# Performance work log

Hardware: AMD Instinct MI355X
Metric: run time of the kernel (lower is better)

## Reference

```python
import jax, jax.numpy as jnp
import numpy as np
from jax import lax

BIN_NUM = 48
CPG = BIN_NUM * 3            # 144 hidden channels
NOUT = BIN_NUM + 1           # 49 symbols
K = 5                        # masked conv kernel size
H, W = 256, 512
TABLE_TOTAL = 65536.0        # EntropyTable total frequency
SCALE = 2.0 / (BIN_NUM - 1.0)


def _causal_mask(include_center: bool) -> jnp.ndarray:
    # Raster-scan causal 5x5 mask: all rows above center, left of center in
    # center row; center tap only for 'hidden' (mask-B) layers.
    m = np.zeros((K, K), np.float32)
    c = K // 2
    m[:c, :] = 1.0
    m[c, :c] = 1.0
    if include_center:
        m[c, c] = 1.0
    return jnp.asarray(m)[None, None]  # broadcast over (O, I, kh, kw)


def _mconv(x, w, b, mask):
    # x: (N, C, H, W); w: (O, I, K, K)
    y = lax.conv_general_dilated(
        x, w * mask, window_strides=(1, 1), padding='SAME',
        dimension_numbers=('NCHW', 'OIHW', 'NCHW'))
    return y + b[None, :, None, None]


def setup_inputs() -> dict:
    key = jax.random.key(0)
    ks = jax.random.split(key, 8)
    # quantized code indices in [0, BIN_NUM)
    data = jax.random.randint(ks[0], (1, 1, H, W), 0, BIN_NUM).astype(jnp.float32)
    s0 = 1.0 / np.sqrt(1 * K * K)
    sr = 1.0 / np.sqrt(CPG * K * K)
    w0 = jax.random.normal(ks[1], (CPG, 1, K, K), jnp.float32) * s0
    b0 = jnp.zeros((CPG,), jnp.float32)
    # 5 residual blocks x 2 convs = 10 hidden masked convs, stacked
    wres = jax.random.normal(ks[2], (10, CPG, CPG, K, K), jnp.float32) * sr
    bres = jnp.zeros((10, CPG), jnp.float32)
    wl = jax.random.normal(ks[3], (NOUT, CPG, K, K), jnp.float32) * sr
    bl = jnp.zeros((NOUT,), jnp.float32)
    return {"data": data, "w0": w0, "b0": b0, "wres": wres, "bres": bres,
            "wl": wl, "bl": bl}


def reference(data, w0, b0, wres, bres, wl, bl):
    mask_a = _causal_mask(False)   # first layer excludes center pixel
    mask_b = _causal_mask(True)    # hidden layers include center pixel

    # Scale(-1, 2/(bin_num-1)): map codes [0, bin_num-1] -> [-1, 1]
    x = data * SCALE - 1.0
    x = jax.nn.relu(_mconv(x, w0, b0, mask_a))
    # 5 residual blocks: y = relu(conv(relu(conv(x)))) + x
    for i in range(5):
        h1 = jax.nn.relu(_mconv(x, wres[2 * i], bres[2 * i], mask_b))
        h2 = jax.nn.relu(_mconv(h1, wres[2 * i + 1], bres[2 * i + 1], mask_b))
        x = x + h2
    logits = _mconv(x, wl, bl, mask_b)          # (1, 49, H, W)

    # EntropyTable: per-pixel softmax -> cumulative frequency table (total 65536)
    probs = jax.nn.softmax(logits, axis=1)
    cdf = jnp.cumsum(probs, axis=1) * TABLE_TOTAL
    zeros = jnp.zeros((cdf.shape[0], 1) + cdf.shape[2:], cdf.dtype)
    vec = jnp.concatenate([zeros, cdf], axis=1)  # (1, 50, H, W)
    return vec
```

## Files before the change

kernel.cpp:

```cpp
#include <hip/hip_runtime.h>

#define HH 256
#define WW 512
#define CPG 144
#define NCO 192
#define NKG 18
#define WP 516
#define HPADR 258
#define XB_E ((size_t)NKG * HPADR * WP * 8)
#define NCH 59
#define KREAL 1872
#define SCALE_F (2.0f / 47.0f)

typedef __attribute__((ext_vector_type(8))) short short8;
typedef __attribute__((ext_vector_type(4))) float floatx4;

__device__ __forceinline__ unsigned short f2bf(float f) {
    unsigned u = __builtin_bit_cast(unsigned, f);
    u += 0x7FFFu + ((u >> 16) & 1u);
    return (unsigned short)(u >> 16);
}
__device__ __forceinline__ float bf2f(unsigned short h) {
    unsigned u = ((unsigned)h) << 16;
    return __builtin_bit_cast(float, u);
}
__device__ __forceinline__ void async16(const void* g, void* l) {
    __builtin_amdgcn_global_load_lds(
        (const __attribute__((address_space(1))) unsigned int*)g,
        (__attribute__((address_space(3))) unsigned int*)l, 16, 0, 0);
}
__device__ __forceinline__ void tap_decode(int t, int& kh, int& kw) {
    kh = t < 5 ? 0 : (t < 10 ? 1 : 2);
    kw = t - (t < 5 ? 0 : (t < 10 ? 5 : 10));
}
__device__ __forceinline__ unsigned aoff68(int c, int lg) {
    int g = c * 4 + lg;
    if (g > 233) g = 233;
    int t = (g * 57) >> 10;
    int kgp = g - t * 18;
    int kh, kw; tap_decode(t, kh, kw);
    return (unsigned)(((kgp * 4 + kh) * 68 + kw) * 16);
}
__device__ __forceinline__ unsigned aoff132(int c, int lg) {
    int g = c * 4 + lg;
    if (g > 233) g = 233;
    int t = (g * 57) >> 10;
    int kgp = g - t * 18;
    int kh, kw; tap_decode(t, kh, kw);
    return (unsigned)(((kgp * 4 + kh) * 132 + kw) * 16);
}

__global__ void k_zero(float* __restrict__ p, size_t n4) {
    size_t i = (size_t)blockIdx.x * blockDim.x + threadIdx.x;
    size_t stride = (size_t)gridDim.x * blockDim.x;
    float4 z = make_float4(0.f, 0.f, 0.f, 0.f);
    for (; i < n4; i += stride) ((float4*)p)[i] = z;
}

__global__ void k_pack_hidden(const float* __restrict__ wres, unsigned short* __restrict__ wpk) {
    const int total = 10 * NCH * NCO * 32;
    int i = blockIdx.x * blockDim.x + threadIdx.x;
    int stride = gridDim.x * blockDim.x;
    for (; i < total; i += stride) {
        int kk = i & 31;
        int q  = i >> 5;
        int co = q % NCO;  q /= NCO;
        int c  = q % NCH;
        int l  = q / NCH;
        int K = c * 32 + kk;
        float v = 0.f;
        if (K < KREAL && co < CPG) {
            int t = K / CPG, ci = K - t * CPG;
            int kh, kw; tap_decode(t, kh, kw);
            v = wres[(((size_t)(l * CPG + co) * CPG + ci) * 5 + kh) * 5 + kw];
        }
        wpk[i] = f2bf(v);
    }
}
__global__ void k_pack_final(const float* __restrict__ wl, unsigned short* __restrict__ wpkF) {
    const int total = NCH * 64 * 32;
    int i = blockIdx.x * blockDim.x + threadIdx.x;
    if (i >= total) return;
    int kk = i & 31;
    int co = (i >> 5) & 63;
    int c  = i >> 11;
    int K = c * 32 + kk;
    float v = 0.f;
    if (K < KREAL && co < 49) {
        int t = K / CPG, ci = K - t * CPG;
        int kh, kw; tap_decode(t, kh, kw);
        v = wl[(((size_t)co * CPG + ci) * 5 + kh) * 5 + kw];
    }
    wpkF[i] = f2bf(v);
}
__global__ void k_pack_small(const float* __restrict__ w0, const float* __restrict__ bl,
                             float* __restrict__ w0p, float* __restrict__ blp) {
    int i = blockIdx.x * blockDim.x + threadIdx.x;
    if (i < 12 * CPG) {
        int co = i % CPG, t = i / CPG;
        int kh, kw; tap_decode(t, kh, kw);
        w0p[i] = w0[co * 25 + kh * 5 + kw];
    } else if (i < 12 * CPG + 64) {
        int k = i - 12 * CPG;
        blp[k] = k < 49 ? bl[k] : 0.f;
    }
}

__global__ __launch_bounds__(384) void k_layer0(
    const float* __restrict__ data, const float* __restrict__ w0p,
    const float* __restrict__ b0, unsigned short* __restrict__ Xb) {
    const int lane = threadIdx.x;
    const int x = blockIdx.x * 64 + lane;
    const int y = blockIdx.y;

    float xv[12];
#pragma unroll
    for (int t = 0; t < 12; t++) {
        int kh, kw; tap_decode(t, kh, kw);
        int yy = y + kh - 2, xx = x + kw - 2;
        xv[t] = (yy >= 0 && xx >= 0 && xx < WW) ? data[yy * WW + xx] * SCALE_F - 1.0f : 0.f;
    }
#pragma unroll
    for (int kgi = 0; kgi < 3; kgi++) {
        int kg = threadIdx.y * 3 + kgi;
        float a8[8];
#pragma unroll
        for (int j = 0; j < 8; j++) a8[j] = 0.f;
#pragma unroll
        for (int t = 0; t < 12; t++)
#pragma unroll
            for (int j = 0; j < 8; j++)
                a8[j] = fmaf(w0p[t * CPG + kg * 8 + j], xv[t], a8[j]);
        short8 o;
#pragma unroll
        for (int j = 0; j < 8; j++)
            o[j] = (short)f2bf(fmaxf(a8[j] + b0[kg * 8 + j], 0.f));
        *(short8*)&Xb[((size_t)(kg * HPADR + y + 2) * WP + (x + 2)) * 8] = o;
    }
}

template<bool RES>
__global__ __launch_bounds__(512, 4) void k_conv(
    const unsigned short* __restrict__ in,
    const unsigned short* __restrict__ wq,
    const float* __restrict__ bias,
    const unsigned short* __restrict__ res,
    unsigned short* __restrict__ out) {
    __shared__ __align__(16) unsigned short As[NKG][4][68][8];
    const int tid  = threadIdx.x;
    const int lane = tid & 63;
    const int wid  = tid >> 6;
    const int ng   = wid & 3;
    const int r    = wid >> 2;
    const int lr = lane & 15;
    const int lg = lane >> 4;

    const int fid = blockIdx.x + (int)gridDim.x * blockIdx.y;
    const int swz = (fid & 7) * 128 + (fid >> 3);
    const int x0 = (swz & 7) * 64;
    const int y0 = (swz >> 3) * 2;

    floatx4 acc[4][3];
#pragma unroll
    for (int m = 0; m < 4; m++)
#pragma unroll
        for (int n = 0; n < 3; n++) acc[m][n] = (floatx4)0.f;

    for (int i = wid; i < 72; i += 8) {
        int rr = i & 3;
        int kg = i >> 2;
        async16(in + ((size_t)(kg * HPADR + y0 + rr) * WP + x0 + lane) * 8,
                &As[kg][rr][0][0]);
    }
    if (tid < 288) {
        int kg = tid >> 4;
        int rr = (tid >> 2) & 3;
        int p  = tid & 3;
        *(short8*)&As[kg][rr][64 + p][0] =
            *(const short8*)(in + ((size_t)(kg * HPADR + y0 + rr) * WP + x0 + 64 + p) * 8);
    }
    asm volatile("s_waitcnt vmcnt(0) lgkmcnt(0)" ::: "memory");
    __builtin_amdgcn_s_barrier();
    __builtin_amdgcn_sched_barrier(0);

    const char* abase = (const char*)As + ((size_t)(r * 68) + lr) * 16;
    auto LDA = [&](int c, short8 (&a)[4]) {
        const char* ap = abase + aoff68(c, lg);
#pragma unroll
        for (int m = 0; m < 4; ++m) a[m] = *(const short8*)(ap + m * 256);
    };
    auto LDB = [&](int c, short8 (&b)[3]) {
        const unsigned short* bp = wq + (size_t)c * (NCO * 32) + (ng * 48 + lr) * 32 + lg * 8;
#pragma unroll
        for (int n = 0; n < 3; ++n) b[n] = *(const short8*)(bp + n * 512);
    };
    auto CMP = [&](const short8 (&a)[4], const short8 (&b)[3]) {
        __builtin_amdgcn_sched_barrier(0);
        __builtin_amdgcn_s_setprio(1);
#pragma unroll
        for (int m = 0; m < 4; ++m)
#pragma unroll
            for (int n = 0; n < 3; ++n)
                acc[m][n] = __builtin_amdgcn_mfma_f32_16x16x32_bf16(a[m], b[n], acc[m][n], 0, 0, 0);
        __builtin_amdgcn_s_setprio(0);
        __builtin_amdgcn_sched_barrier(0);
    };

    short8 A0[4], A1[4], B0[3], B1[3];
    LDB(0, B0); LDA(0, A0);
#pragma unroll 1
    for (int c = 0; c < 56; c += 2) {
        LDB(c + 1, B1); LDA(c + 1, A1);
        CMP(A0, B0);
        LDB(c + 2, B0); LDA(c + 2, A0);
        CMP(A1, B1);
    }
    LDB(57, B1); LDA(57, A1);
    CMP(A0, B0);
    LDB(58, B0); LDA(58, A0);
    CMP(A1, B1);
    CMP(A0, B0);

    if (ng < 3) {
#pragma unroll
        for (int n = 0; n < 3; ++n) {
            int co = ng * 48 + n * 16 + lr;
            float bv = bias[co];
            const size_t pb = ((size_t)((co >> 3) * HPADR + y0 + 2 + r) * WP + (x0 + 2)) * 8 + (co & 7);
#pragma unroll
            for (int m = 0; m < 4; ++m)
#pragma unroll
                for (int rr = 0; rr < 4; ++rr) {
                    int px = m * 16 + lg * 4 + rr;
                    size_t o = pb + (size_t)px * 8;
                    float v = fmaxf(acc[m][n][rr] + bv, 0.f);
                    if (RES) v += bf2f(res[o]);
                    out[o] = f2bf(v);
                }
        }
    }
}

__global__ __launch_bounds__(512, 2) void k_logits(
    const unsigned short* __restrict__ in,
    const unsigned short* __restrict__ wq,
    const float* __restrict__ blp,
    float* __restrict__ logits) {
    __shared__ __align__(16) unsigned short As[NKG][4][132][8];
    const int tid  = threadIdx.x;
    const int lane = tid & 63;
    const int wid  = tid >> 6;
    const int ng   = wid & 1;
    const int r    = (wid >> 1) & 1;
    const int ph   = wid >> 2;
    const int lr = lane & 15;
    const int lg = lane >> 4;

    const int fid = blockIdx.x + (int)gridDim.x * blockIdx.y;
    const int swz = (fid & 7) * 64 + (fid >> 3);
    const int x0 = (swz & 3) * 128;
    const int y0 = (swz >> 2) * 2;

    floatx4 acc[4][2];
#pragma unroll
    for (int m = 0; m < 4; m++)
#pragma unroll
        for (int n = 0; n < 2; n++) acc[m][n] = (floatx4)0.f;

    for (int i = wid; i < 144; i += 8) {
        int half = i & 1;
        int rr   = (i >> 1) & 3;
        int kg   = i >> 3;
        async16(in + ((size_t)(kg * HPADR + y0 + rr) * WP + x0 + half * 64 + lane) * 8,
                &As[kg][rr][half * 64][0]);
    }
    if (tid < 288) {
        int kg = tid >> 4;
        int rr = (tid >> 2) & 3;
        int pxl = 128 + (tid & 3);
        *(short8*)&As[kg][rr][pxl][0] =
            *(const short8*)(in + ((size_t)(kg * HPADR + y0 + rr) * WP + x0 + pxl) * 8);
    }
    asm volatile("s_waitcnt vmcnt(0) lgkmcnt(0)" ::: "memory");
    __builtin_amdgcn_s_barrier();
    __builtin_amdgcn_sched_barrier(0);

    const char* abase = (const char*)As + ((size_t)(r * 132) + ph * 64 + lr) * 16;
    auto LDA = [&](int c, short8 (&a)[4]) {
        const char* ap = abase + aoff132(c, lg);
#pragma unroll
        for (int m = 0; m < 4; ++m) a[m] = *(const short8*)(ap + m * 256);
    };
    auto LDB = [&](int c, short8 (&b)[2]) {
        const unsigned short* bp = wq + (size_t)c * 2048 + (ng * 32 + lr) * 32 + lg * 8;
#pragma unroll
        for (int n = 0; n < 2; ++n) b[n] = *(const short8*)(bp + n * 512);
    };
    auto CMP = [&](const short8 (&a)[4], const short8 (&b)[2]) {
        __builtin_amdgcn_sched_barrier(0);
        __builtin_amdgcn_s_setprio(1);
#pragma unroll
        for (int m = 0; m < 4; ++m)
#pragma unroll
            for (int n = 0; n < 2; ++n)
                acc[m][n] = __builtin_amdgcn_mfma_f32_16x16x32_bf16(a[m], b[n], acc[m][n], 0, 0, 0);
        __builtin_amdgcn_s_setprio(0);
        __builtin_amdgcn_sched_barrier(0);
    };

    short8 A0[4], A1[4], B0[2], B1[2], B2[2], B3[2];
    LDB(0, B0); LDB(1, B1); LDA(0, A0);
#pragma unroll 1
    for (int c = 0; c < 56; c += 4) {
        LDB(c + 2, B2); LDB(c + 3, B3);
        LDA(c + 1, A1); CMP(A0, B0);
        LDA(c + 2, A0); CMP(A1, B1);
        LDB(c + 4, B0); LDB(c + 5, B1);
        LDA(c + 3, A1); CMP(A0, B2);
        LDA(c + 4, A0); CMP(A1, B3);
    }
    LDB(58, B2);
    LDA(57, A1); CMP(A0, B0);
    LDA(58, A0); CMP(A1, B1);
    CMP(A0, B2);

#pragma unroll
    for (int n = 0; n < 2; ++n) {
        int co = ng * 32 + n * 16 + lr;
        float bv = blp[co];
#pragma unroll
        for (int m = 0; m < 4; ++m)
#pragma unroll
            for (int rr = 0; rr < 4; ++rr) {
                int px = ph * 64 + m * 16 + lg * 4 + rr;
                logits[((size_t)(y0 + r) * WW + x0 + px) * 64 + co] = acc[m][n][rr] + bv;
            }
    }
}

__global__ __launch_bounds__(256) void k_softmax(
    const float* __restrict__ lg, float* __restrict__ out) {
    const int px = blockIdx.x * 256 + threadIdx.x;
    const int y = blockIdx.y;
    const size_t p = (size_t)y * WW + px;
    const float* l = lg + p * 64;
    float v[49];
    float m = -1e30f;
#pragma unroll
    for (int k = 0; k < 49; k++) { v[k] = l[k]; m = fmaxf(m, v[k]); }
    float s = 0.f;
#pragma unroll
    for (int k = 0; k < 49; k++) {
        v[k] = exp2f((v[k] - m) * 1.44269504088896f);
        s += v[k];
    }
    const float inv = 65536.0f / s;
    out[p] = 0.f;
    float run = 0.f;
#pragma unroll
    for (int k = 0; k < 49; k++) {
        run += v[k];
        out[(size_t)(k + 1) * (HH * WW) + p] = run * inv;
    }
}

extern "C" void kernel_launch(void* const* d_in, const int* in_sizes, int n_in,
                              void* d_out, int out_size, void* d_ws, size_t ws_size,
                              hipStream_t stream) {
    (void)in_sizes; (void)n_in; (void)out_size; (void)ws_size;
    const float* data = (const float*)d_in[0];
    const float* w0   = (const float*)d_in[1];
    const float* b0   = (const float*)d_in[2];
    const float* wres = (const float*)d_in[3];
    const float* bres = (const float*)d_in[4];
    const float* wl   = (const float*)d_in[5];
    const float* bl   = (const float*)d_in[6];
    float* out = (float*)d_out;

    char* ws = (char*)d_ws;
    unsigned short* Xb   = (unsigned short*)ws;
    unsigned short* Hb   = Xb + XB_E;
    unsigned short* wpk  = Hb + XB_E;
    unsigned short* wpkF = wpk + (size_t)10 * NCH * NCO * 32;
    float* blp  = (float*)(wpkF + (size_t)NCH * 64 * 32);
    float* w0p  = blp + 64;
    float* logits = w0p + 1728;

    k_zero<<<2048, 256, 0, stream>>>((float*)ws, (2 * XB_E * 2) / 16);

    k_pack_hidden<<<2048, 256, 0, stream>>>(wres, wpk);
    k_pack_final<<<(NCH * 64 * 32 + 255) / 256, 256, 0, stream>>>(wl, wpkF);
    k_pack_small<<<7, 256, 0, stream>>>(w0, bl, w0p, blp);

    k_layer0<<<dim3(8, 256), dim3(64, 6), 0, stream>>>(data, w0p, b0, Xb);

    const size_t LSTRIDE = (size_t)NCH * NCO * 32;
    for (int i = 0; i < 5; i++) {
        k_conv<false><<<dim3(8, 128), 512, 0, stream>>>(
            Xb, wpk + (size_t)(2 * i) * LSTRIDE, bres + (2 * i) * CPG, Xb, Hb);
        k_conv<true><<<dim3(8, 128), 512, 0, stream>>>(
            Hb, wpk + (size_t)(2 * i + 1) * LSTRIDE, bres + (2 * i + 1) * CPG, Xb, Xb);
    }

    k_logits<<<dim3(4, 128), 512, 0, stream>>>(Xb, wpkF, blp, logits);
    k_softmax<<<dim3(2, 256), 256, 0, stream>>>(logits, out);
}
```

Before: 1.046 ms.

## Stage conv weights in LDS ring buffer and enlarge tile to four rows

The hidden-layer conv kernel now covers four output rows per block with twelve waves (768 threads), removing the idle fourth channel-group of waves by dropping the padding to 192 output channels. Weights are repacked without that padding and streamed through a 3-slot LDS ring using async global-to-LDS loads, so waves in a block share the weight reads instead of each fetching from global memory. The cost is a block barrier every K-chunk, more LDS per block and lower occupancy (3 blocks of 768 threads).

```diff
diff --git a/kernel.cpp b/kernel.cpp
--- a/kernel.cpp
+++ b/kernel.cpp
@@ -3,7 +3,6 @@
 #define HH 256
 #define WW 512
 #define CPG 144
-#define NCO 192
 #define NKG 18
 #define WP 516
 #define HPADR 258
@@ -12,6 +11,9 @@
 #define KREAL 1872
 #define SCALE_F (2.0f / 47.0f)
 
+#define BSLAB 1552
+#define BSLOT (4 * BSLAB)
+
 typedef __attribute__((ext_vector_type(8))) short short8;
 typedef __attribute__((ext_vector_type(4))) float floatx4;
 
@@ -33,13 +35,13 @@
     kh = t < 5 ? 0 : (t < 10 ? 1 : 2);
     kw = t - (t < 5 ? 0 : (t < 10 ? 5 : 10));
 }
-__device__ __forceinline__ unsigned aoff68(int c, int lg) {
+__device__ __forceinline__ unsigned aoff6(int c, int lg) {
     int g = c * 4 + lg;
     if (g > 233) g = 233;
     int t = (g * 57) >> 10;
     int kgp = g - t * 18;
     int kh, kw; tap_decode(t, kh, kw);
-    return (unsigned)(((kgp * 4 + kh) * 68 + kw) * 16);
+    return (unsigned)(((kgp * 6 + kh) * 68 + kw) * 16);
 }
 __device__ __forceinline__ unsigned aoff132(int c, int lg) {
     int g = c * 4 + lg;
@@ -58,18 +60,19 @@
 }
 
 __global__ void k_pack_hidden(const float* __restrict__ wres, unsigned short* __restrict__ wpk) {
-    const int total = 10 * NCH * NCO * 32;
+    const int total = 10 * NCH * 4 * CPG * 8;
     int i = blockIdx.x * blockDim.x + threadIdx.x;
     int stride = gridDim.x * blockDim.x;
     for (; i < total; i += stride) {
-        int kk = i & 31;
-        int q  = i >> 5;
-        int co = q % NCO;  q /= NCO;
+        int j  = i & 7;
+        int q  = i >> 3;
+        int co = q % CPG;  q /= CPG;
+        int lg = q & 3;    q >>= 2;
         int c  = q % NCH;
         int l  = q / NCH;
-        int K = c * 32 + kk;
+        int K = c * 32 + lg * 8 + j;
         float v = 0.f;
-        if (K < KREAL && co < CPG) {
+        if (K < KREAL) {
             int t = K / CPG, ci = K - t * CPG;
             int kh, kw; tap_decode(t, kh, kw);
             v = wres[(((size_t)(l * CPG + co) * CPG + ci) * 5 + kh) * 5 + kw];
@@ -140,25 +143,26 @@
 }
 
 template<bool RES>
-__global__ __launch_bounds__(512, 4) void k_conv(
+__global__ __launch_bounds__(768, 3) void k_conv(
     const unsigned short* __restrict__ in,
     const unsigned short* __restrict__ wq,
     const float* __restrict__ bias,
     const unsigned short* __restrict__ res,
     unsigned short* __restrict__ out) {
-    __shared__ __align__(16) unsigned short As[NKG][4][68][8];
+    __shared__ __align__(16) unsigned short As[NKG][6][68][8];
+    __shared__ __align__(16) unsigned short Bs[3][BSLOT];
     const int tid  = threadIdx.x;
     const int lane = tid & 63;
     const int wid  = tid >> 6;
-    const int ng   = wid & 3;
-    const int r    = wid >> 2;
+    const int ng   = wid % 3;
+    const int r    = wid / 3;
     const int lr = lane & 15;
     const int lg = lane >> 4;
 
     const int fid = blockIdx.x + (int)gridDim.x * blockIdx.y;
-    const int swz = (fid & 7) * 128 + (fid >> 3);
+    const int swz = (fid & 7) * 64 + (fid >> 3);
     const int x0 = (swz & 7) * 64;
-    const int y0 = (swz >> 3) * 2;
+    const int y0 = (swz >> 3) * 4;
 
     floatx4 acc[4][3];
 #pragma unroll
@@ -166,33 +170,45 @@
 #pragma unroll
         for (int n = 0; n < 3; n++) acc[m][n] = (floatx4)0.f;
 
-    for (int i = wid; i < 72; i += 8) {
-        int rr = i & 3;
-        int kg = i >> 2;
+    const int lgw = wid >> 2;
+    const int lgs = wid / 3;
+    const int ps  = wid - lgs * 3;
+    (void)lgw;
+    char* bdst = (char*)&Bs[0][0] + lgs * 3104 + ps * 1024;
+    const size_t bsrc = (size_t)lgs * 1152 + (size_t)ps * 512 + (size_t)lane * 8;
+    auto stageB = [&](int c) {
+        async16(wq + (size_t)c * 4608 + bsrc, bdst + (c % 3) * (BSLOT * 2));
+    };
+
+    for (int i = wid; i < 108; i += 12) {
+        int kg = i / 6, rr = i - (i / 6) * 6;
         async16(in + ((size_t)(kg * HPADR + y0 + rr) * WP + x0 + lane) * 8,
                 &As[kg][rr][0][0]);
     }
-    if (tid < 288) {
-        int kg = tid >> 4;
-        int rr = (tid >> 2) & 3;
-        int p  = tid & 3;
+    if (tid < 432) {
+        int kg = tid / 24;
+        int rem = tid - kg * 24;
+        int rr = rem >> 2;
+        int p  = rem & 3;
         *(short8*)&As[kg][rr][64 + p][0] =
             *(const short8*)(in + ((size_t)(kg * HPADR + y0 + rr) * WP + x0 + 64 + p) * 8);
     }
+    stageB(0); stageB(1);
     asm volatile("s_waitcnt vmcnt(0) lgkmcnt(0)" ::: "memory");
     __builtin_amdgcn_s_barrier();
     __builtin_amdgcn_sched_barrier(0);
 
     const char* abase = (const char*)As + ((size_t)(r * 68) + lr) * 16;
+    const char* bbase = (const char*)&Bs[0][0] + (ng * 48 + lr) * 16;
     auto LDA = [&](int c, short8 (&a)[4]) {
-        const char* ap = abase + aoff68(c, lg);
+        const char* ap = abase + aoff6(c, lg);
 #pragma unroll
         for (int m = 0; m < 4; ++m) a[m] = *(const short8*)(ap + m * 256);
     };
-    auto LDB = [&](int c, short8 (&b)[3]) {
-        const unsigned short* bp = wq + (size_t)c * (NCO * 32) + (ng * 48 + lr) * 32 + lg * 8;
-#pragma unroll
-        for (int n = 0; n < 3; ++n) b[n] = *(const short8*)(bp + n * 512);
+    auto LDBl = [&](int c, short8 (&b)[3]) {
+        const char* bp = bbase + (c % 3) * (BSLOT * 2) + lg * 3104;
+#pragma unroll
+        for (int n = 0; n < 3; ++n) b[n] = *(const short8*)(bp + n * 256);
     };
     auto CMP = [&](const short8 (&a)[4], const short8 (&b)[3]) {
         __builtin_amdgcn_sched_barrier(0);
@@ -206,38 +222,57 @@
         __builtin_amdgcn_sched_barrier(0);
     };
 
-    short8 A0[4], A1[4], B0[3], B1[3];
-    LDB(0, B0); LDA(0, A0);
+    short8 A0[4], A1[4], b[3];
+    LDA(0, A0);
 #pragma unroll 1
     for (int c = 0; c < 56; c += 2) {
-        LDB(c + 1, B1); LDA(c + 1, A1);
-        CMP(A0, B0);
-        LDB(c + 2, B0); LDA(c + 2, A0);
-        CMP(A1, B1);
-    }
-    LDB(57, B1); LDA(57, A1);
-    CMP(A0, B0);
-    LDB(58, B0); LDA(58, A0);
-    CMP(A1, B1);
-    CMP(A0, B0);
-
-    if (ng < 3) {
-#pragma unroll
-        for (int n = 0; n < 3; ++n) {
-            int co = ng * 48 + n * 16 + lr;
-            float bv = bias[co];
-            const size_t pb = ((size_t)((co >> 3) * HPADR + y0 + 2 + r) * WP + (x0 + 2)) * 8 + (co & 7);
-#pragma unroll
-            for (int m = 0; m < 4; ++m)
-#pragma unroll
-                for (int rr = 0; rr < 4; ++rr) {
-                    int px = m * 16 + lg * 4 + rr;
-                    size_t o = pb + (size_t)px * 8;
-                    float v = fmaxf(acc[m][n][rr] + bv, 0.f);
-                    if (RES) v += bf2f(res[o]);
-                    out[o] = f2bf(v);
-                }
-        }
+        stageB(c + 2);
+        LDBl(c, b);
+        LDA(c + 1, A1);
+        CMP(A0, b);
+        asm volatile("s_waitcnt vmcnt(1)" ::: "memory");
+        __builtin_amdgcn_s_barrier();
+        __builtin_amdgcn_sched_barrier(0);
+
+        stageB(c + 3);
+        LDBl(c + 1, b);
+        LDA(c + 2, A0);
+        CMP(A1, b);
+        asm volatile("s_waitcnt vmcnt(1)" ::: "memory");
+        __builtin_amdgcn_s_barrier();
+        __builtin_amdgcn_sched_barrier(0);
+    }
+    stageB(58);
+    LDBl(56, b);
+    LDA(57, A1);
+    CMP(A0, b);
+    asm volatile("s_waitcnt vmcnt(1)" ::: "memory");
+    __builtin_amdgcn_s_barrier();
+    __builtin_amdgcn_sched_barrier(0);
+    LDBl(57, b);
+    LDA(58, A0);
+    CMP(A1, b);
+    asm volatile("s_waitcnt vmcnt(0)" ::: "memory");
+    __builtin_amdgcn_s_barrier();
+    __builtin_amdgcn_sched_barrier(0);
+    LDBl(58, b);
+    CMP(A0, b);
+
+#pragma unroll
+    for (int n = 0; n < 3; ++n) {
+        int co = ng * 48 + n * 16 + lr;
+        float bv = bias[co];
+        const size_t pb = ((size_t)((co >> 3) * HPADR + y0 + 2 + r) * WP + (x0 + 2)) * 8 + (co & 7);
+#pragma unroll
+        for (int m = 0; m < 4; ++m)
+#pragma unroll
+            for (int rr = 0; rr < 4; ++rr) {
+                int px = m * 16 + lg * 4 + rr;
+                size_t o = pb + (size_t)px * 8;
+                float v = fmaxf(acc[m][n][rr] + bv, 0.f);
+                if (RES) v += bf2f(res[o]);
+                out[o] = f2bf(v);
+            }
     }
 }
 
@@ -381,7 +416,7 @@
     unsigned short* Xb   = (unsigned short*)ws;
     unsigned short* Hb   = Xb + XB_E;
     unsigned short* wpk  = Hb + XB_E;
-    unsigned short* wpkF = wpk + (size_t)10 * NCH * NCO * 32;
+    unsigned short* wpkF = wpk + (size_t)10 * NCH * 4 * CPG * 8;
     float* blp  = (float*)(wpkF + (size_t)NCH * 64 * 32);
     float* w0p  = blp + 64;
     float* logits = w0p + 1728;
@@ -394,11 +429,11 @@
 
     k_layer0<<<dim3(8, 256), dim3(64, 6), 0, stream>>>(data, w0p, b0, Xb);
 
-    const size_t LSTRIDE = (size_t)NCH * NCO * 32;
+    const size_t LSTRIDE = (size_t)NCH * 4 * CPG * 8;
     for (int i = 0; i < 5; i++) {
-        k_conv<false><<<dim3(8, 128), 512, 0, stream>>>(
+        k_conv<false><<<dim3(8, 64), 768, 0, stream>>>(
             Xb, wpk + (size_t)(2 * i) * LSTRIDE, bres + (2 * i) * CPG, Xb, Hb);
-        k_conv<true><<<dim3(8, 128), 512, 0, stream>>>(
+        k_conv<true><<<dim3(8, 64), 768, 0, stream>>>(
             Hb, wpk + (size_t)(2 * i + 1) * LSTRIDE, bres + (2 * i + 1) * CPG, Xb, Xb);
     }
 
```

Result: slower. 1.146 ms (+9.6%).
